# Kernel tuning notes

Measured on AMD Instinct MI355X. Metric: run time of the kernel, lower is better.

## Reference

```python
import jax, jax.numpy as jnp
import numpy as np

B, T, C, H = 8, 2048, 1024, 128

def setup_inputs() -> dict:
    key = jax.random.key(0)
    k1, k2, k3, k4 = jax.random.split(key, 4)
    scale = 0.02
    return {
        "x": jax.random.normal(k1, (B, T, C), dtype=jnp.float32),
        "Wq": jax.random.normal(k2, (C, H), dtype=jnp.float32) * scale,
        "Wk": jax.random.normal(k3, (C, H), dtype=jnp.float32) * scale,
        "Wv": jax.random.normal(k4, (C, H), dtype=jnp.float32) * scale,
    }

def reference(x, Wq, Wk, Wv):
    # Single causal attention head (dropout p=0.0 -> identity)
    q = jnp.einsum('btc,ch->bth', x, Wq)
    k = jnp.einsum('btc,ch->bth', x, Wk)
    v = jnp.einsum('btc,ch->bth', x, Wv)
    head_size = k.shape[-1]
    scores = jnp.einsum('bth,bsh->bts', q, k) / jnp.sqrt(jnp.asarray(head_size, q.dtype))  # [B,T,T]
    causal = jnp.tril(jnp.ones((scores.shape[1], scores.shape[2]), dtype=bool))
    scores = jnp.where(causal, scores, -jnp.inf)
    weights = jax.nn.softmax(scores, axis=-1)
    context = jnp.einsum('bts,bsh->bth', weights, v)  # [B,T,H]
    return context
```

## Files before the change

### kernel.cpp

```cpp
#include <hip/hip_runtime.h>

typedef __bf16 bf16x8 __attribute__((ext_vector_type(8)));
typedef float f32x4 __attribute__((ext_vector_type(4)));
typedef float fv4 __attribute__((ext_vector_type(4)));

#define B_ 8
#define T_ 2048
#define C_ 1024
#define H_ 128

__device__ __forceinline__ void gload16(void* lds, const void* g) {
  __builtin_amdgcn_global_load_lds(
      (const __attribute__((address_space(1))) void*)g,
      (__attribute__((address_space(3))) void*)lds, 16, 0, 0);
}


__global__ __launch_bounds__(256) void prep_kernel(
    const float* __restrict__ Wq, const float* __restrict__ Wk,
    const float* __restrict__ Wv, __bf16* __restrict__ Wt)
{
  __shared__ __bf16 ldsT[128 * 136];
  const int tid = threadIdx.x;
  const int k0 = blockIdx.x * 128;
  const int wsel = blockIdx.y;
  const float* W = wsel == 0 ? Wq : (wsel == 1 ? Wk : Wv);
#pragma unroll
  for (int i = 0; i < 16; ++i) {
    int fidx = tid + 256 * i;
    int k = fidx >> 5, h4 = (fidx & 31) << 2;
    fv4 w = *(const fv4*)(W + (size_t)(k0 + k) * H_ + h4);
#pragma unroll
    for (int j = 0; j < 4; ++j) ldsT[(h4 + j) * 136 + k] = (__bf16)w[j];
  }
  __syncthreads();
#pragma unroll
  for (int i = 0; i < 8; ++i) {
    int sidx = tid + 256 * i;
    int h = sidx >> 4, c8 = (sidx & 15) << 3;
    *(bf16x8*)(Wt + (size_t)wsel * H_ * C_ + (size_t)h * C_ + k0 + c8) =
        *(const bf16x8*)&ldsT[h * 136 + c8];
  }
}

__global__ __launch_bounds__(512) void proj_kernel(
    const float* __restrict__ x, const __bf16* __restrict__ Wt,
    __bf16* __restrict__ Qw, __bf16* __restrict__ Kw, __bf16* __restrict__ Vtw)
{
  __shared__ __align__(16) float ldsA[2][64 * 64];
  __shared__ __align__(16) __bf16 ldsB[2][192 * 64];
  const int tid = threadIdx.x;
  const int wave = tid >> 6, lane = tid & 63;
  const int q4 = lane >> 4, l16 = lane & 15;
  const int wm = wave >> 2, wn = wave & 3;
  const int bt0 = blockIdx.x * 64;
  const int cb0 = blockIdx.y * 192;

  const int arow = tid >> 4, agx = tid & 15;
  const int bcol = tid >> 3, bgx = tid & 7;

  const f32x4 zero4 = {0.f, 0.f, 0.f, 0.f};
  f32x4 acc[2][3];
#pragma unroll
  for (int mt = 0; mt < 2; ++mt)
#pragma unroll
    for (int nt = 0; nt < 3; ++nt) acc[mt][nt] = zero4;

  auto stage = [&](int bufi, int k0) {
#pragma unroll
    for (int i = 0; i < 2; ++i) {
      int row = i * 32 + arow;
      gload16((char*)&ldsA[bufi][0] + i * 8192 + wave * 1024,
              x + (size_t)(bt0 + row) * C_ + k0 + ((agx ^ (row & 7)) << 2));
    }
#pragma unroll
    for (int i = 0; i < 3; ++i) {
      int col = i * 64 + bcol;
      gload16((char*)&ldsB[bufi][0] + i * 8192 + wave * 1024,
              Wt + (size_t)(cb0 + col) * C_ + k0 + ((bgx ^ (col & 7)) << 3));
    }
  };

  stage(0, 0);
  stage(1, 64);

  for (int it = 0; it < 16; ++it) {
    const int buf = it & 1;
    if (it < 15) asm volatile("s_waitcnt vmcnt(5)" ::: "memory");
    else         asm volatile("s_waitcnt vmcnt(0)" ::: "memory");
    __builtin_amdgcn_sched_barrier(0);
    __builtin_amdgcn_s_barrier();
    __builtin_amdgcn_sched_barrier(0);
#pragma unroll
    for (int kc = 0; kc < 2; ++kc) {
      bf16x8 af[2];
#pragma unroll
      for (int mt = 0; mt < 2; ++mt) {
        const int rl = wm * 32 + mt * 16 + l16;
        const int rx = rl & 7;
        fv4 a0 = *(const fv4*)&ldsA[buf][rl * 64 + (((kc * 8 + q4 * 2 + 0) ^ rx) << 2)];
        fv4 a1 = *(const fv4*)&ldsA[buf][rl * 64 + (((kc * 8 + q4 * 2 + 1) ^ rx) << 2)];
#pragma unroll
        for (int j = 0; j < 4; ++j) { af[mt][j] = (__bf16)a0[j]; af[mt][4 + j] = (__bf16)a1[j]; }
      }
#pragma unroll
      for (int nt = 0; nt < 3; ++nt) {
        const int cl = wn * 48 + nt * 16 + l16;
        bf16x8 bf = *(const bf16x8*)&ldsB[buf][cl * 64 + (((kc * 4 + q4) ^ (cl & 7)) << 3)];
#pragma unroll
        for (int mt = 0; mt < 2; ++mt)
          acc[mt][nt] = __builtin_amdgcn_mfma_f32_16x16x32_bf16(af[mt], bf, acc[mt][nt], 0, 0, 0);
      }
    }
    __builtin_amdgcn_sched_barrier(0);
    __builtin_amdgcn_s_barrier();
    __builtin_amdgcn_sched_barrier(0);
    if (it + 2 < 16) stage(buf, (it + 2) * 64);
  }

  const int b = bt0 >> 11, t0 = bt0 & (T_ - 1);
  __bf16* ldsV = (__bf16*)&ldsB[0][0];
#pragma unroll
  for (int mt = 0; mt < 2; ++mt)
#pragma unroll
    for (int nt = 0; nt < 3; ++nt) {
      int gcol = cb0 + wn * 48 + nt * 16 + l16;
#pragma unroll
      for (int r = 0; r < 4; ++r) {
        int tl = wm * 32 + mt * 16 + q4 * 4 + r;
        float v = acc[mt][nt][r];
        if (gcol < 128) Qw[(size_t)(bt0 + tl) * H_ + gcol] = (__bf16)v;
        else if (gcol < 256) Kw[(size_t)(bt0 + tl) * H_ + (gcol - 128)] = (__bf16)v;
        else ldsV[(gcol - 256) * 72 + tl] = (__bf16)v;
      }
    }
  if (cb0 == 192) {
    __syncthreads();
#pragma unroll
    for (int i = 0; i < 2; ++i) {
      int idx = tid + 512 * i;
      int h = idx >> 3, t8 = (idx & 7) << 3;
      *(bf16x8*)(Vtw + ((size_t)b * H_ + h) * T_ + t0 + t8) =
          *(const bf16x8*)&ldsV[h * 72 + t8];
    }
  }
}

__global__ __launch_bounds__(256) void attn_split(
    const __bf16* __restrict__ Q, const __bf16* __restrict__ K,
    const __bf16* __restrict__ Vt, __bf16* __restrict__ PO,
    float* __restrict__ Pl, float* __restrict__ out)
{
  __shared__ __align__(16) __bf16 ldsK[2][32 * 128];
  __shared__ __align__(16) __bf16 ldsV[2][128 * 32];
  __shared__ __align__(16) __bf16 ldsP[4][16 * 40];
  const int tid = threadIdx.x;
  const int wave = tid >> 6, lane = tid & 63;
  const int q4 = lane >> 4, l16 = lane & 15;
  const int flat = blockIdx.x;
  const int b = flat & 7;
  int rem = flat >> 3, qb = 0;
  while (rem >= (qb >> 3) + 1) { rem -= (qb >> 3) + 1; ++qb; }
  const int c = rem;
  const int tstart = c << 3;
  const int tend = min(tstart + 8, qb + 1);
  const int nst = 2 * (tend - tstart);
  const int nch = (qb >> 3) + 1;
  const int qw = qb * 64 + wave * 16;
  const __bf16* Qb = Q + (size_t)b * T_ * H_;
  const __bf16* Kb = K + (size_t)b * T_ * H_;
  const __bf16* Vb = Vt + (size_t)b * H_ * T_;
  __bf16* ldsPw = &ldsP[wave][0];

  bf16x8 qf[4];
#pragma unroll
  for (int kc = 0; kc < 4; ++kc)
    qf[kc] = *(const bf16x8*)(Qb + (size_t)(qw + l16) * H_ + kc * 32 + q4 * 8);

  const f32x4 zero4 = {0.f, 0.f, 0.f, 0.f};
  f32x4 o[8];
#pragma unroll
  for (int nt = 0; nt < 8; ++nt) o[nt] = zero4;
  float lsum[4] = {0.f, 0.f, 0.f, 0.f};

  auto stageKV = [&](int bufi, int kv0) {
#pragma unroll
    for (int i = 0; i < 2; ++i) {
      int idx = tid + 256 * i;
      int kr = idx >> 4, kg = idx & 15;
      gload16((char*)&ldsK[bufi][0] + i * 4096 + wave * 1024,
              Kb + (size_t)(kv0 + kr) * H_ + ((kg ^ (kr & 7)) << 3));
      int vr = idx >> 2, vg = idx & 3;
      gload16((char*)&ldsV[bufi][0] + i * 4096 + wave * 1024,
              Vb + (size_t)vr * T_ + kv0 + ((vg ^ ((vr >> 1) & 3)) << 3));
    }
  };

  const int kvbase = tstart << 6;
  stageKV(0, kvbase);
  stageKV(1, kvbase + 32);

  for (int ht = 0; ht < nst; ++ht) {
    const int buf = ht & 1;
    const int kv0 = kvbase + ht * 32;
    if (ht + 1 < nst) asm volatile("s_waitcnt vmcnt(4)" ::: "memory");
    else              asm volatile("s_waitcnt vmcnt(0)" ::: "memory");
    __builtin_amdgcn_sched_barrier(0);
    __builtin_amdgcn_s_barrier();
    __builtin_amdgcn_sched_barrier(0);

    f32x4 s[2];
    s[0] = zero4; s[1] = zero4;
#pragma unroll
    for (int nt2 = 0; nt2 < 2; ++nt2) {
      const int krow = nt2 * 16 + l16;
      const int kx = krow & 7;
#pragma unroll
      for (int kc = 0; kc < 4; ++kc) {
        bf16x8 kf = *(const bf16x8*)&ldsK[buf][krow * 128 + (((kc * 4 + q4) ^ kx) << 3)];
        s[nt2] = __builtin_amdgcn_mfma_f32_16x16x32_bf16(qf[kc], kf, s[nt2], 0, 0, 0);
      }
    }

    if ((kv0 >> 6) == qb) {
#pragma unroll
      for (int r = 0; r < 4; ++r) {
        const int grow = qw + q4 * 4 + r;
#pragma unroll
        for (int nt2 = 0; nt2 < 2; ++nt2) {
          int col = kv0 + nt2 * 16 + l16;
          float p = (col <= grow) ? __expf(s[nt2][r] * 0.08838834764831845f) : 0.f;
          lsum[r] += p;
          ldsPw[(q4 * 4 + r) * 40 + nt2 * 16 + l16] = (__bf16)p;
        }
      }
    } else {
#pragma unroll
      for (int r = 0; r < 4; ++r)
#pragma unroll
        for (int nt2 = 0; nt2 < 2; ++nt2) {
          float p = __expf(s[nt2][r] * 0.08838834764831845f);
          lsum[r] += p;
          ldsPw[(q4 * 4 + r) * 40 + nt2 * 16 + l16] = (__bf16)p;
        }
    }

    bf16x8 pf = *(const bf16x8*)&ldsPw[l16 * 40 + q4 * 8];
#pragma unroll
    for (int nt = 0; nt < 8; ++nt) {
      const int vrow = nt * 16 + l16;
      bf16x8 vf = *(const bf16x8*)&ldsV[buf][vrow * 32 + ((q4 ^ ((vrow >> 1) & 3)) << 3)];
      o[nt] = __builtin_amdgcn_mfma_f32_16x16x32_bf16(pf, vf, o[nt], 0, 0, 0);
    }
    __builtin_amdgcn_sched_barrier(0);
    __builtin_amdgcn_s_barrier();
    __builtin_amdgcn_sched_barrier(0);
    if (ht + 2 < nst) stageKV(buf, kv0 + 64);
  }

  float lred[4];
#pragma unroll
  for (int r = 0; r < 4; ++r) {
    float l = lsum[r];
    l += __shfl_xor(l, 1);
    l += __shfl_xor(l, 2);
    l += __shfl_xor(l, 4);
    l += __shfl_xor(l, 8);
    lred[r] = l;
  }

  if (nch == 1) {
#pragma unroll
    for (int r = 0; r < 4; ++r) lred[r] = 1.f / lred[r];
#pragma unroll
    for (int nt = 0; nt < 8; ++nt)
#pragma unroll
      for (int r = 0; r < 4; ++r) {
        int row = qw + q4 * 4 + r;
        out[((size_t)b * T_ + row) * H_ + nt * 16 + l16] = o[nt][r] * lred[r];
      }
  } else {
    const int slot = b * 80 + qb + max(qb - 8, 0) + max(qb - 16, 0) + max(qb - 24, 0) + c;
    __bf16* POs = PO + (size_t)slot * 8192;
#pragma unroll
    for (int nt = 0; nt < 8; ++nt)
#pragma unroll
      for (int r = 0; r < 4; ++r)
        POs[(wave * 16 + q4 * 4 + r) * 128 + nt * 16 + l16] = (__bf16)o[nt][r];
    if (l16 == 0)
#pragma unroll
      for (int r = 0; r < 4; ++r)
        Pl[slot * 64 + wave * 16 + q4 * 4 + r] = lred[r];
  }
}

__global__ __launch_bounds__(256) void attn_combine(
    const __bf16* __restrict__ PO, const float* __restrict__ Pl,
    float* __restrict__ out)
{
  const int flat = blockIdx.x;
  const int b = flat & 7;
  const int rest = flat >> 3;
  const int qb = 8 + (rest >> 2);
  const int seg = rest & 3;
  const int nch = (qb >> 3) + 1;
  const int slot0 = b * 80 + qb + max(qb - 8, 0) + max(qb - 16, 0) + max(qb - 24, 0);
  const int tid = threadIdx.x;
  const int rloc = seg * 16 + (tid >> 4);
  const int col8 = (tid & 15) << 3;
  float oacc[8] = {0.f};
  float lacc = 0.f;
  for (int cc = 0; cc < nch; ++cc) {
    const int slot = slot0 + cc;
    lacc += Pl[slot * 64 + rloc];
    bf16x8 v = *(const bf16x8*)(PO + (size_t)slot * 8192 + rloc * 128 + col8);
#pragma unroll
    for (int j = 0; j < 8; ++j) oacc[j] += (float)v[j];
  }
  const float inv = 1.f / lacc;
  float* op = out + ((size_t)b * T_ + qb * 64 + rloc) * H_ + col8;
  fv4 v0, v1;
#pragma unroll
  for (int j = 0; j < 4; ++j) { v0[j] = oacc[j] * inv; v1[j] = oacc[4 + j] * inv; }
  *(fv4*)op = v0;
  *(fv4*)(op + 4) = v1;
}

__global__ __launch_bounds__(256) void attn_mono(
    const __bf16* __restrict__ Q, const __bf16* __restrict__ K,
    const __bf16* __restrict__ Vt, float* __restrict__ out)
{
  __shared__ __align__(16) __bf16 ldsK[64 * 136];
  __shared__ __align__(16) __bf16 ldsV[128 * 72];
  __shared__ __align__(16) __bf16 ldsP[4][16 * 72];
  const int tid = threadIdx.x;
  const int wave = tid >> 6, lane = tid & 63;
  const int q4 = lane >> 4, l16 = lane & 15;
  const int qb = blockIdx.x, b = blockIdx.y;
  const int qw = qb * 64 + wave * 16;
  const __bf16* Qb = Q + (size_t)b * T_ * H_;
  const __bf16* Kb = K + (size_t)b * T_ * H_;
  const __bf16* Vb = Vt + (size_t)b * H_ * T_;
  __bf16* ldsPw = &ldsP[wave][0];

  bf16x8 qf[4];
#pragma unroll
  for (int kc = 0; kc < 4; ++kc)
    qf[kc] = *(const bf16x8*)(Qb + (size_t)(qw + l16) * H_ + kc * 32 + q4 * 8);

  const f32x4 zero4 = {0.f, 0.f, 0.f, 0.f};
  f32x4 o[8];
#pragma unroll
  for (int nt = 0; nt < 8; ++nt) o[nt] = zero4;
  float lsum[4] = {0.f, 0.f, 0.f, 0.f};
  const int ntile = qb + 1;

  bf16x8 kp[4], vp[4];
#pragma unroll
  for (int i = 0; i < 4; ++i) {
    int idx = tid + 256 * i;
    int krow = idx >> 4, kcol8 = (idx & 15) << 3;
    kp[i] = *(const bf16x8*)(Kb + (size_t)krow * H_ + kcol8);
    int vrow = idx >> 3, vcol8 = (idx & 7) << 3;
    vp[i] = *(const bf16x8*)(Vb + (size_t)vrow * T_ + vcol8);
  }

  for (int t = 0; t < ntile; ++t) {
    const int kv0 = t << 6;
#pragma unroll
    for (int i = 0; i < 4; ++i) {
      int idx = tid + 256 * i;
      int krow = idx >> 4, kcol8 = (idx & 15) << 3;
      *(bf16x8*)&ldsK[krow * 136 + kcol8] = kp[i];
      int vrow = idx >> 3, vcol8 = (idx & 7) << 3;
      *(bf16x8*)&ldsV[vrow * 72 + vcol8] = vp[i];
    }
    __syncthreads();
    int kvn = (t + 1 < ntile) ? (kv0 + 64) : kv0;
#pragma unroll
    for (int i = 0; i < 4; ++i) {
      int idx = tid + 256 * i;
      int krow = idx >> 4, kcol8 = (idx & 15) << 3;
      kp[i] = *(const bf16x8*)(Kb + (size_t)(kvn + krow) * H_ + kcol8);
      int vrow = idx >> 3, vcol8 = (idx & 7) << 3;
      vp[i] = *(const bf16x8*)(Vb + (size_t)vrow * T_ + kvn + vcol8);
    }
    f32x4 s[4];
#pragma unroll
    for (int nt = 0; nt < 4; ++nt) s[nt] = zero4;
#pragma unroll
    for (int nt = 0; nt < 4; ++nt)
#pragma unroll
      for (int kc = 0; kc < 4; ++kc) {
        bf16x8 kf = *(const bf16x8*)&ldsK[(nt * 16 + l16) * 136 + kc * 32 + q4 * 8];
        s[nt] = __builtin_amdgcn_mfma_f32_16x16x32_bf16(qf[kc], kf, s[nt], 0, 0, 0);
      }
#pragma unroll
    for (int r = 0; r < 4; ++r) {
      const int grow = qw + q4 * 4 + r;
#pragma unroll
      for (int nt = 0; nt < 4; ++nt) {
        int col = kv0 + nt * 16 + l16;
        float p = (col <= grow) ? __expf(s[nt][r] * 0.08838834764831845f) : 0.f;
        lsum[r] += p;
        ldsPw[(q4 * 4 + r) * 72 + nt * 16 + l16] = (__bf16)p;
      }
    }
#pragma unroll
    for (int kc2 = 0; kc2 < 2; ++kc2) {
      bf16x8 pf = *(const bf16x8*)&ldsPw[l16 * 72 + kc2 * 32 + q4 * 8];
#pragma unroll
      for (int nt = 0; nt < 8; ++nt) {
        bf16x8 vf = *(const bf16x8*)&ldsV[(nt * 16 + l16) * 72 + kc2 * 32 + q4 * 8];
        o[nt] = __builtin_amdgcn_mfma_f32_16x16x32_bf16(pf, vf, o[nt], 0, 0, 0);
      }
    }
    __syncthreads();
  }
  float rinv[4];
#pragma unroll
  for (int r = 0; r < 4; ++r) {
    float l = lsum[r];
    l += __shfl_xor(l, 1);
    l += __shfl_xor(l, 2);
    l += __shfl_xor(l, 4);
    l += __shfl_xor(l, 8);
    rinv[r] = 1.f / l;
  }
#pragma unroll
  for (int nt = 0; nt < 8; ++nt)
#pragma unroll
    for (int r = 0; r < 4; ++r) {
      int row = qw + q4 * 4 + r;
      out[((size_t)b * T_ + row) * H_ + nt * 16 + l16] = o[nt][r] * rinv[r];
    }
}

extern "C" void kernel_launch(void* const* d_in, const int* in_sizes, int n_in,
                              void* d_out, int out_size, void* d_ws, size_t ws_size,
                              hipStream_t stream) {
  const float* x  = (const float*)d_in[0];
  const float* Wq = (const float*)d_in[1];
  const float* Wk = (const float*)d_in[2];
  const float* Wv = (const float*)d_in[3];
  __bf16* ws = (__bf16*)d_ws;
  __bf16* Qw  = ws;
  __bf16* Kw  = ws + (size_t)B_ * T_ * H_;
  __bf16* Vtw = ws + (size_t)2 * B_ * T_ * H_;
  __bf16* Wt  = ws + (size_t)3 * B_ * T_ * H_;
  const size_t bf16_elems = 6684672;
  __bf16* PO = ws + bf16_elems;
  float* Pl = (float*)(ws + bf16_elems + (size_t)640 * 8192);
  const size_t need = bf16_elems * 2 + (size_t)640 * 8192 * 2 + (size_t)640 * 64 * 4;
  float* out = (float*)d_out;

  prep_kernel<<<dim3(8, 3), 256, 0, stream>>>(Wq, Wk, Wv, Wt);
  proj_kernel<<<dim3(256, 2), 512, 0, stream>>>(x, Wt, Qw, Kw, Vtw);
  if (ws_size >= need) {
    attn_split<<<640, 256, 0, stream>>>(Qw, Kw, Vtw, PO, Pl, out);
    attn_combine<<<768, 256, 0, stream>>>(PO, Pl, out);
  } else {
    attn_mono<<<dim3(32, 8), 256, 0, stream>>>(Qw, Kw, Vtw, out);
  }
}
```

Measured before the change: 149.8 us.

## Double query rows per split-attention block to reuse K/V tiles across two M-tiles

Each wave now handles 32 query rows (two 16-row MFMA tiles) instead of 16, so a block covers 128 queries. Each K/V tile staged in LDS feeds twice as many MFMAs, and the grid for the split kernel halves. Waves also skip the QK and PV work for KV tiles that lie entirely above their causal diagonal. The partial-output slot layout and the combine kernel are re-indexed to match. The cost is doubled accumulator registers and fewer blocks across the CUs, which may hurt occupancy and load balance.

```diff
diff --git a/kernel.cpp b/kernel.cpp
--- a/kernel.cpp
+++ b/kernel.cpp
@@ -153,35 +153,39 @@
 {
   __shared__ __align__(16) __bf16 ldsK[2][32 * 128];
   __shared__ __align__(16) __bf16 ldsV[2][128 * 32];
-  __shared__ __align__(16) __bf16 ldsP[4][16 * 40];
+  __shared__ __align__(16) __bf16 ldsP[4][32 * 40];
   const int tid = threadIdx.x;
   const int wave = tid >> 6, lane = tid & 63;
   const int q4 = lane >> 4, l16 = lane & 15;
   const int flat = blockIdx.x;
   const int b = flat & 7;
-  int rem = flat >> 3, qb = 0;
-  while (rem >= (qb >> 3) + 1) { rem -= (qb >> 3) + 1; ++qb; }
+  int rem = flat >> 3, qb2 = 0;
+  while (rem >= (qb2 >> 2) + 1) { rem -= (qb2 >> 2) + 1; ++qb2; }
   const int c = rem;
   const int tstart = c << 3;
-  const int tend = min(tstart + 8, qb + 1);
+  const int tend = min(tstart + 8, 2 * qb2 + 2);
   const int nst = 2 * (tend - tstart);
-  const int nch = (qb >> 3) + 1;
-  const int qw = qb * 64 + wave * 16;
+  const int nch = (qb2 >> 2) + 1;
+  const int qw = qb2 * 128 + wave * 32;
   const __bf16* Qb = Q + (size_t)b * T_ * H_;
   const __bf16* Kb = K + (size_t)b * T_ * H_;
   const __bf16* Vb = Vt + (size_t)b * H_ * T_;
   __bf16* ldsPw = &ldsP[wave][0];
 
-  bf16x8 qf[4];
-#pragma unroll
-  for (int kc = 0; kc < 4; ++kc)
-    qf[kc] = *(const bf16x8*)(Qb + (size_t)(qw + l16) * H_ + kc * 32 + q4 * 8);
+  bf16x8 qf[2][4];
+#pragma unroll
+  for (int qm = 0; qm < 2; ++qm)
+#pragma unroll
+    for (int kc = 0; kc < 4; ++kc)
+      qf[qm][kc] = *(const bf16x8*)(Qb + (size_t)(qw + qm * 16 + l16) * H_ + kc * 32 + q4 * 8);
 
   const f32x4 zero4 = {0.f, 0.f, 0.f, 0.f};
-  f32x4 o[8];
-#pragma unroll
-  for (int nt = 0; nt < 8; ++nt) o[nt] = zero4;
-  float lsum[4] = {0.f, 0.f, 0.f, 0.f};
+  f32x4 o[2][8];
+#pragma unroll
+  for (int qm = 0; qm < 2; ++qm)
+#pragma unroll
+    for (int nt = 0; nt < 8; ++nt) o[qm][nt] = zero4;
+  float lsum[2][4] = {{0.f, 0.f, 0.f, 0.f}, {0.f, 0.f, 0.f, 0.f}};
 
   auto stageKV = [&](int bufi, int kv0) {
 #pragma unroll
@@ -209,88 +213,114 @@
     __builtin_amdgcn_s_barrier();
     __builtin_amdgcn_sched_barrier(0);
 
-    f32x4 s[2];
-    s[0] = zero4; s[1] = zero4;
-#pragma unroll
-    for (int nt2 = 0; nt2 < 2; ++nt2) {
-      const int krow = nt2 * 16 + l16;
-      const int kx = krow & 7;
-#pragma unroll
-      for (int kc = 0; kc < 4; ++kc) {
-        bf16x8 kf = *(const bf16x8*)&ldsK[buf][krow * 128 + (((kc * 4 + q4) ^ kx) << 3)];
-        s[nt2] = __builtin_amdgcn_mfma_f32_16x16x32_bf16(qf[kc], kf, s[nt2], 0, 0, 0);
-      }
-    }
-
-    if ((kv0 >> 6) == qb) {
-#pragma unroll
-      for (int r = 0; r < 4; ++r) {
-        const int grow = qw + q4 * 4 + r;
-#pragma unroll
-        for (int nt2 = 0; nt2 < 2; ++nt2) {
-          int col = kv0 + nt2 * 16 + l16;
-          float p = (col <= grow) ? __expf(s[nt2][r] * 0.08838834764831845f) : 0.f;
-          lsum[r] += p;
-          ldsPw[(q4 * 4 + r) * 40 + nt2 * 16 + l16] = (__bf16)p;
+    if (kv0 < qw + 32) {
+      f32x4 s[2][2];
+      s[0][0] = zero4; s[0][1] = zero4; s[1][0] = zero4; s[1][1] = zero4;
+#pragma unroll
+      for (int nt2 = 0; nt2 < 2; ++nt2) {
+        const int krow = nt2 * 16 + l16;
+        const int kx = krow & 7;
+#pragma unroll
+        for (int kc = 0; kc < 4; ++kc) {
+          bf16x8 kf = *(const bf16x8*)&ldsK[buf][krow * 128 + (((kc * 4 + q4) ^ kx) << 3)];
+#pragma unroll
+          for (int qm = 0; qm < 2; ++qm)
+            s[qm][nt2] = __builtin_amdgcn_mfma_f32_16x16x32_bf16(qf[qm][kc], kf, s[qm][nt2], 0, 0, 0);
         }
       }
-    } else {
-#pragma unroll
-      for (int r = 0; r < 4; ++r)
-#pragma unroll
-        for (int nt2 = 0; nt2 < 2; ++nt2) {
-          float p = __expf(s[nt2][r] * 0.08838834764831845f);
-          lsum[r] += p;
-          ldsPw[(q4 * 4 + r) * 40 + nt2 * 16 + l16] = (__bf16)p;
+
+      if (kv0 + 31 > qw) {
+#pragma unroll
+        for (int qm = 0; qm < 2; ++qm)
+#pragma unroll
+          for (int r = 0; r < 4; ++r) {
+            const int grow = qw + qm * 16 + q4 * 4 + r;
+#pragma unroll
+            for (int nt2 = 0; nt2 < 2; ++nt2) {
+              int col = kv0 + nt2 * 16 + l16;
+              float p = (col <= grow) ? __expf(s[qm][nt2][r] * 0.08838834764831845f) : 0.f;
+              lsum[qm][r] += p;
+              ldsPw[(qm * 16 + q4 * 4 + r) * 40 + nt2 * 16 + l16] = (__bf16)p;
+            }
+          }
+      } else {
+#pragma unroll
+        for (int qm = 0; qm < 2; ++qm)
+#pragma unroll
+          for (int r = 0; r < 4; ++r)
+#pragma unroll
+            for (int nt2 = 0; nt2 < 2; ++nt2) {
+              float p = __expf(s[qm][nt2][r] * 0.08838834764831845f);
+              lsum[qm][r] += p;
+              ldsPw[(qm * 16 + q4 * 4 + r) * 40 + nt2 * 16 + l16] = (__bf16)p;
+            }
+      }
+
+      bf16x8 pf[2];
+#pragma unroll
+      for (int qm = 0; qm < 2; ++qm)
+        pf[qm] = *(const bf16x8*)&ldsPw[(qm * 16 + l16) * 40 + q4 * 8];
+#pragma unroll
+      for (int nt = 0; nt < 8; ++nt) {
+        const int vrow = nt * 16 + l16;
+        bf16x8 vf = *(const bf16x8*)&ldsV[buf][vrow * 32 + ((q4 ^ ((vrow >> 1) & 3)) << 3)];
+#pragma unroll
+        for (int qm = 0; qm < 2; ++qm)
+          o[qm][nt] = __builtin_amdgcn_mfma_f32_16x16x32_bf16(pf[qm], vf, o[qm][nt], 0, 0, 0);
+      }
+    }
+    __builtin_amdgcn_sched_barrier(0);
+    __builtin_amdgcn_s_barrier();
+    __builtin_amdgcn_sched_barrier(0);
+    if (ht + 2 < nst) stageKV(buf, kv0 + 64);
+  }
+
+  float lred[2][4];
+#pragma unroll
+  for (int qm = 0; qm < 2; ++qm)
+#pragma unroll
+    for (int r = 0; r < 4; ++r) {
+      float l = lsum[qm][r];
+      l += __shfl_xor(l, 1);
+      l += __shfl_xor(l, 2);
+      l += __shfl_xor(l, 4);
+      l += __shfl_xor(l, 8);
+      lred[qm][r] = l;
+    }
+
+  if (nch == 1) {
+#pragma unroll
+    for (int qm = 0; qm < 2; ++qm)
+#pragma unroll
+      for (int r = 0; r < 4; ++r) lred[qm][r] = 1.f / lred[qm][r];
+#pragma unroll
+    for (int qm = 0; qm < 2; ++qm)
+#pragma unroll
+      for (int nt = 0; nt < 8; ++nt)
+#pragma unroll
+        for (int r = 0; r < 4; ++r) {
+          int row = qw + qm * 16 + q4 * 4 + r;
+          out[((size_t)b * T_ + row) * H_ + nt * 16 + l16] = o[qm][nt][r] * lred[qm][r];
         }
-    }
-
-    bf16x8 pf = *(const bf16x8*)&ldsPw[l16 * 40 + q4 * 8];
-#pragma unroll
-    for (int nt = 0; nt < 8; ++nt) {
-      const int vrow = nt * 16 + l16;
-      bf16x8 vf = *(const bf16x8*)&ldsV[buf][vrow * 32 + ((q4 ^ ((vrow >> 1) & 3)) << 3)];
-      o[nt] = __builtin_amdgcn_mfma_f32_16x16x32_bf16(pf, vf, o[nt], 0, 0, 0);
-    }
-    __builtin_amdgcn_sched_barrier(0);
-    __builtin_amdgcn_s_barrier();
-    __builtin_amdgcn_sched_barrier(0);
-    if (ht + 2 < nst) stageKV(buf, kv0 + 64);
-  }
-
-  float lred[4];
-#pragma unroll
-  for (int r = 0; r < 4; ++r) {
-    float l = lsum[r];
-    l += __shfl_xor(l, 1);
-    l += __shfl_xor(l, 2);
-    l += __shfl_xor(l, 4);
-    l += __shfl_xor(l, 8);
-    lred[r] = l;
-  }
-
-  if (nch == 1) {
-#pragma unroll
-    for (int r = 0; r < 4; ++r) lred[r] = 1.f / lred[r];
-#pragma unroll
-    for (int nt = 0; nt < 8; ++nt)
-#pragma unroll
-      for (int r = 0; r < 4; ++r) {
-        int row = qw + q4 * 4 + r;
-        out[((size_t)b * T_ + row) * H_ + nt * 16 + l16] = o[nt][r] * lred[r];
-      }
   } else {
-    const int slot = b * 80 + qb + max(qb - 8, 0) + max(qb - 16, 0) + max(qb - 24, 0) + c;
-    __bf16* POs = PO + (size_t)slot * 8192;
-#pragma unroll
-    for (int nt = 0; nt < 8; ++nt)
-#pragma unroll
-      for (int r = 0; r < 4; ++r)
-        POs[(wave * 16 + q4 * 4 + r) * 128 + nt * 16 + l16] = (__bf16)o[nt][r];
+    int off = 2 * (qb2 - 4);
+    if (qb2 >= 8)  off = 8 + 3 * (qb2 - 8);
+    if (qb2 >= 12) off = 20 + 4 * (qb2 - 12);
+    const int slot = b * 36 + off + c;
+    __bf16* POs = PO + (size_t)slot * 16384;
+#pragma unroll
+    for (int qm = 0; qm < 2; ++qm)
+#pragma unroll
+      for (int nt = 0; nt < 8; ++nt)
+#pragma unroll
+        for (int r = 0; r < 4; ++r)
+          POs[(wave * 32 + qm * 16 + q4 * 4 + r) * 128 + nt * 16 + l16] = (__bf16)o[qm][nt][r];
     if (l16 == 0)
 #pragma unroll
-      for (int r = 0; r < 4; ++r)
-        Pl[slot * 64 + wave * 16 + q4 * 4 + r] = lred[r];
+      for (int qm = 0; qm < 2; ++qm)
+#pragma unroll
+        for (int r = 0; r < 4; ++r)
+          Pl[slot * 128 + wave * 32 + qm * 16 + q4 * 4 + r] = lred[qm][r];
   }
 }
 
@@ -301,10 +331,13 @@
   const int flat = blockIdx.x;
   const int b = flat & 7;
   const int rest = flat >> 3;
-  const int qb = 8 + (rest >> 2);
-  const int seg = rest & 3;
-  const int nch = (qb >> 3) + 1;
-  const int slot0 = b * 80 + qb + max(qb - 8, 0) + max(qb - 16, 0) + max(qb - 24, 0);
+  const int qb2 = 4 + (rest >> 3);
+  const int seg = rest & 7;
+  const int nch = (qb2 >> 2) + 1;
+  int off = 2 * (qb2 - 4);
+  if (qb2 >= 8)  off = 8 + 3 * (qb2 - 8);
+  if (qb2 >= 12) off = 20 + 4 * (qb2 - 12);
+  const int slot0 = b * 36 + off;
   const int tid = threadIdx.x;
   const int rloc = seg * 16 + (tid >> 4);
   const int col8 = (tid & 15) << 3;
@@ -312,13 +345,13 @@
   float lacc = 0.f;
   for (int cc = 0; cc < nch; ++cc) {
     const int slot = slot0 + cc;
-    lacc += Pl[slot * 64 + rloc];
-    bf16x8 v = *(const bf16x8*)(PO + (size_t)slot * 8192 + rloc * 128 + col8);
+    lacc += Pl[slot * 128 + rloc];
+    bf16x8 v = *(const bf16x8*)(PO + (size_t)slot * 16384 + rloc * 128 + col8);
 #pragma unroll
     for (int j = 0; j < 8; ++j) oacc[j] += (float)v[j];
   }
   const float inv = 1.f / lacc;
-  float* op = out + ((size_t)b * T_ + qb * 64 + rloc) * H_ + col8;
+  float* op = out + ((size_t)b * T_ + qb2 * 128 + rloc) * H_ + col8;
   fv4 v0, v1;
 #pragma unroll
   for (int j = 0; j < 4; ++j) { v0[j] = oacc[j] * inv; v1[j] = oacc[4 + j] * inv; }
@@ -450,14 +483,14 @@
   __bf16* Wt  = ws + (size_t)3 * B_ * T_ * H_;
   const size_t bf16_elems = 6684672;
   __bf16* PO = ws + bf16_elems;
-  float* Pl = (float*)(ws + bf16_elems + (size_t)640 * 8192);
-  const size_t need = bf16_elems * 2 + (size_t)640 * 8192 * 2 + (size_t)640 * 64 * 4;
+  float* Pl = (float*)(ws + bf16_elems + (size_t)288 * 16384);
+  const size_t need = bf16_elems * 2 + (size_t)288 * 16384 * 2 + (size_t)288 * 128 * 4;
   float* out = (float*)d_out;
 
   prep_kernel<<<dim3(8, 3), 256, 0, stream>>>(Wq, Wk, Wv, Wt);
   proj_kernel<<<dim3(256, 2), 512, 0, stream>>>(x, Wt, Qw, Kw, Vtw);
   if (ws_size >= need) {
-    attn_split<<<640, 256, 0, stream>>>(Qw, Kw, Vtw, PO, Pl, out);
+    attn_split<<<320, 256, 0, stream>>>(Qw, Kw, Vtw, PO, Pl, out);
     attn_combine<<<768, 256, 0, stream>>>(PO, Pl, out);
   } else {
     attn_mono<<<dim3(32, 8), 256, 0, stream>>>(Qw, Kw, Vtw, out);
```

After: 156.2 us. 1.04x slower.
